# Kernel tuning notes

Hardware: AMD Instinct MI355X
Metric: run time of the kernel (lower is better)

The kernel has to match this reference:

```python
import jax, jax.numpy as jnp
import numpy as np

B, H, S, D = 2, 16, 2048, 64
DROPOUT_P = 0.1
INV_SCALE = 8.0  # sqrt(D), original: q.size(3) * k.size(-1)**-0.5


def setup_inputs() -> dict:
    key = jax.random.key(0)
    kq, kk, kv, km = jax.random.split(key, 4)
    query = jax.random.normal(kq, (B, H, S, D), dtype=jnp.float32)
    k_ = jax.random.normal(kk, (B, H, S, D), dtype=jnp.float32)
    value = jax.random.normal(kv, (B, H, S, D), dtype=jnp.float32)
    keep = jax.random.bernoulli(km, 1.0 - DROPOUT_P, (B, H, S, S))
    # torch train-mode dropout: keep-mask scaled by 1/(1-p)
    dropout_mask = keep.astype(jnp.float32) / (1.0 - DROPOUT_P)
    return {"query": query, "key": k_, "value": value, "dropout_mask": dropout_mask}


def reference(query, key, value, dropout_mask):
    # qk = q @ k^T, scaled by 1/sqrt(D)
    scores = jnp.einsum("bhqd,bhkd->bhqk", query, key) / INV_SCALE
    probs = jax.nn.softmax(scores, axis=-1)
    probs = probs * dropout_mask  # deterministic dropout
    out = jnp.einsum("bhqk,bhkd->bhqd", probs, value)
    return out
```

## Files before the change

### kernel.cpp

```cpp
#include <hip/hip_runtime.h>
#include <hip/hip_bf16.h>

typedef __attribute__((ext_vector_type(4))) float f32x4;
typedef __attribute__((ext_vector_type(8))) short s16x8;
typedef __attribute__((ext_vector_type(4))) short s16x4;

constexpr int S    = 2048;
constexpr int D    = 64;
constexpr int BH   = 32;
constexpr int QBLK = 64;
constexpr int KBLK = 32;
constexpr int NSL  = S / KBLK;

__device__ __forceinline__ short f2bf(float f) {
  union { float f; unsigned u; } x;
  x.f = f;
  unsigned r = x.u + 0x7fffu + ((x.u >> 16) & 1u);
  return (short)(r >> 16);
}

typedef const __attribute__((address_space(1))) unsigned int* as1_u32p;
typedef __attribute__((address_space(3))) unsigned int* as3_u32p;

__global__ __launch_bounds__(256) void prepass(const float* __restrict__ K,
                                               const float* __restrict__ V,
                                               short* __restrict__ Kb,
                                               short* __restrict__ Vt) {
  const int bid = blockIdx.x;
  const int tid = threadIdx.x;
  if (bid < BH * 32) {
    const int bh = bid >> 5, sl = bid & 31;
    const float* src = K + ((size_t)bh * S + (size_t)sl * 64) * D;
    short* dst = Kb + ((size_t)bh * S + (size_t)sl * 64) * D;
    #pragma unroll
    for (int c = 0; c < 2; ++c) {
      const int idx = tid * 2 + c;
      const int row = idx >> 3;
      const int ch  = idx & 7;
      const float* s = src + row * D + ch * 8;
      f32x4 a = *(const f32x4*)s, b = *(const f32x4*)(s + 4);
      s16x8 o;
      #pragma unroll
      for (int j = 0; j < 4; ++j) { o[j] = f2bf(a[j]); o[4 + j] = f2bf(b[j]); }
      *(s16x8*)(dst + row * D + ((ch ^ (row & 7)) * 8)) = o;
    }
  } else {
    __shared__ short tile[32][72];
    const int b2 = bid - BH * 32;
    const int bh = b2 >> 6, sl = b2 & 63;
    const float* src = V + ((size_t)bh * S + (size_t)sl * 32) * D;
    {
      const int row = tid >> 3;
      const int c0  = (tid & 7) * 8;
      f32x4 a = *(const f32x4*)(src + row * D + c0);
      f32x4 b = *(const f32x4*)(src + row * D + c0 + 4);
      #pragma unroll
      for (int j = 0; j < 4; ++j) {
        tile[row][c0 + j]     = f2bf(a[j]);
        tile[row][c0 + 4 + j] = f2bf(b[j]);
      }
    }
    __syncthreads();
    short* dst = Vt + ((size_t)bh * 64 + sl) * (D * KBLK);
    const int d = tid >> 2, c = tid & 3;
    const int pos = c ^ ((d >> 1) & 3);
    s16x8 o;
    #pragma unroll
    for (int j = 0; j < 8; ++j) o[j] = tile[c * 8 + j][d];
    *(s16x8*)(dst + d * KBLK + pos * 8) = o;
  }
}

__global__ __launch_bounds__(256, 4)
void attn_fwd4(const float* __restrict__ Qg, const short* __restrict__ Kb,
               const short* __restrict__ Vt, const float* __restrict__ Mg,
               float* __restrict__ Og) {
  __shared__ alignas(16) short K_lds[3][KBLK][64];
  __shared__ alignas(16) short V_lds[3][D][KBLK];
  __shared__ alignas(16) short P_lds[4][16][KBLK];

  const int tid  = threadIdx.x;
  const int wave = tid >> 6;
  const int lane = tid & 63;
  const int lq   = lane & 15;
  const int g    = lane >> 4;

  const int bh = blockIdx.x & (BH - 1);
  const int qt = blockIdx.x / BH;
  const size_t base = (size_t)bh * S * D;
  const int    qrow = qt * QBLK + wave * 16 + lq;
  const float* mrow = Mg + ((size_t)bh * S + qrow) * S + g * 4;

  s16x8 qf[2];
  {
    const float sc = 1.44269504088896340736f * 0.125f;
    const float* qp = Qg + base + (size_t)qrow * D + g * 8;
    #pragma unroll
    for (int h = 0; h < 2; ++h) {
      f32x4 a = *(const f32x4*)(qp + h * 32);
      f32x4 b = *(const f32x4*)(qp + h * 32 + 4);
      #pragma unroll
      for (int j = 0; j < 4; ++j) {
        qf[h][j]     = f2bf(a[j] * sc);
        qf[h][4 + j] = f2bf(b[j] * sc);
      }
    }
  }

  f32x4 acc[4];
  #pragma unroll
  for (int dt = 0; dt < 4; ++dt) acc[dt] = (f32x4)0.0f;
  float m = -1e30f, lp = 0.0f;

  const char* kbase = (const char*)(Kb + base);
  const char* vbase = (const char*)(Vt + (size_t)bh * 64 * (D * KBLK));
  char* kl = (char*)&K_lds[0][0][0];
  char* vl = (char*)&V_lds[0][0][0];
  char* pl = (char*)&P_lds[wave][lq][0];

  auto stageKV = [&](int buf, int it) {
    __builtin_amdgcn_global_load_lds((as1_u32p)(kbase + (size_t)it * 4096 + wave * 1024 + lane * 16),
                                     (as3_u32p)(kl + buf * 4096 + wave * 1024 + lane * 16), 16, 0, 0);
    __builtin_amdgcn_global_load_lds((as1_u32p)(vbase + (size_t)it * 4096 + wave * 1024 + lane * 16),
                                     (as3_u32p)(vl + buf * 4096 + wave * 1024 + lane * 16), 16, 0, 0);
  };
  auto loadM = [&](int it, f32x4* mk) {
    const float* mp = mrow + it * KBLK;
    mk[0] = *(const f32x4*)(mp);
    mk[1] = *(const f32x4*)(mp + 16);
  };

  auto body = [&](int it, int cur, f32x4* mkU, f32x4* mkN) {
    {
      int nb = cur + 2; if (nb >= 3) nb -= 3;
      if (it + 2 < NSL) stageKV(nb, it + 2);
      if (it + 1 < NSL) loadM(it + 1, mkN);
    }

    f32x4 st[2];
    __builtin_amdgcn_s_setprio(1);
    #pragma unroll
    for (int t = 0; t < 2; ++t) {
      st[t] = (f32x4)0.0f;
      #pragma unroll
      for (int h = 0; h < 2; ++h) {
        const s16x8 kf = *(const s16x8*)(kl + cur * 4096 + (t * 16 + lq) * 128 +
                                         (((h * 4 + g) ^ (lq & 7)) * 16));
        st[t] = __builtin_amdgcn_mfma_f32_16x16x32_bf16(kf, qf[h], st[t], 0, 0, 0);
      }
    }
    __builtin_amdgcn_s_setprio(0);

    const float mx = fmaxf(fmaxf(fmaxf(st[0][0], st[0][1]), fmaxf(st[0][2], st[0][3])),
                           fmaxf(fmaxf(st[1][0], st[1][1]), fmaxf(st[1][2], st[1][3])));
    if (!__all(mx <= m + 8.0f)) {
      float rm = fmaxf(mx, __shfl_xor(mx, 16));
      rm = fmaxf(rm, __shfl_xor(rm, 32));
      const float mn  = fmaxf(m, rm);
      const float fac = __builtin_amdgcn_exp2f(m - mn);
      lp *= fac;
      #pragma unroll
      for (int dt = 0; dt < 4; ++dt)
        #pragma unroll
        for (int r = 0; r < 4; ++r) acc[dt][r] *= fac;
      m = mn;
    }
    float p[8];
    #pragma unroll
    for (int t = 0; t < 2; ++t)
      #pragma unroll
      for (int r = 0; r < 4; ++r) p[t * 4 + r] = __builtin_amdgcn_exp2f(st[t][r] - m);
    lp += ((p[0] + p[1]) + (p[2] + p[3])) + ((p[4] + p[5]) + (p[6] + p[7]));

    #pragma unroll
    for (int t = 0; t < 2; ++t) {
      s16x4 pk;
      #pragma unroll
      for (int r = 0; r < 4; ++r) pk[r] = f2bf(p[t * 4 + r] * mkU[t][r]);
      *(s16x4*)(pl + (((2 * t + (g >> 1)) ^ ((lq >> 1) & 3)) * 16) + (g & 1) * 8) = pk;
    }
    asm volatile("" ::: "memory");

    const s16x8 pf = *(const s16x8*)(pl + ((g ^ ((lq >> 1) & 3)) * 16));
    __builtin_amdgcn_s_setprio(1);
    #pragma unroll
    for (int dt = 0; dt < 4; ++dt) {
      const s16x8 vf = *(const s16x8*)(vl + cur * 4096 + (dt * 16 + lq) * 64 +
                                       ((g ^ ((lq >> 1) & 3)) * 16));
      acc[dt] = __builtin_amdgcn_mfma_f32_16x16x32_bf16(vf, pf, acc[dt], 0, 0, 0);
    }
    __builtin_amdgcn_s_setprio(0);

    asm volatile("s_waitcnt vmcnt(4)" ::: "memory");
    __builtin_amdgcn_s_barrier();
    __builtin_amdgcn_sched_barrier(0);
  };

  f32x4 mkA[2], mkB[2];
  stageKV(0, 0);
  stageKV(1, 1);
  loadM(0, mkA);
  asm volatile("s_waitcnt vmcnt(4)" ::: "memory");
  __builtin_amdgcn_s_barrier();
  __builtin_amdgcn_sched_barrier(0);

  int cur = 0;
  #pragma unroll 1
  for (int it = 0; it < NSL; it += 2) {
    body(it,     cur, mkA, mkB); cur = (cur == 2) ? 0 : cur + 1;
    body(it + 1, cur, mkB, mkA); cur = (cur == 2) ? 0 : cur + 1;
  }

  float l = lp + __shfl_xor(lp, 16);
  l += __shfl_xor(l, 32);
  const float inv_l = 1.0f / l;
  float* op = Og + base + (size_t)qrow * D;
  #pragma unroll
  for (int dt = 0; dt < 4; ++dt) {
    f32x4 o;
    #pragma unroll
    for (int r = 0; r < 4; ++r) o[r] = acc[dt][r] * inv_l;
    *(f32x4*)(op + dt * 16 + g * 4) = o;
  }
}

__global__ __launch_bounds__(256, 4)
void attn_fwd_fb(const float* __restrict__ Qg, const float* __restrict__ Kg,
                 const float* __restrict__ Vg, const float* __restrict__ Mg,
                 float* __restrict__ Og) {
  __shared__ alignas(16) short Kl[32][72];
  __shared__ alignas(16) short Vl[D][40];
  __shared__ alignas(16) short Pl[4][16][40];
  const int tid = threadIdx.x, wave = tid >> 6, lane = tid & 63;
  const int lq = lane & 15, g = lane >> 4;
  const int bh = blockIdx.x & (BH - 1), qt = blockIdx.x / BH;
  const size_t base = (size_t)bh * S * D;
  const int qrow = qt * QBLK + wave * 16 + lq;
  const float* mrow = Mg + ((size_t)bh * S + qrow) * S;
  s16x8 qf[2];
  {
    const float sc = 1.44269504088896340736f * 0.125f;
    const float* qp = Qg + base + (size_t)qrow * D + g * 8;
    #pragma unroll
    for (int h = 0; h < 2; ++h) {
      f32x4 a = *(const f32x4*)(qp + h * 32);
      f32x4 b = *(const f32x4*)(qp + h * 32 + 4);
      #pragma unroll
      for (int j = 0; j < 4; ++j) { qf[h][j] = f2bf(a[j] * sc); qf[h][4 + j] = f2bf(b[j] * sc); }
    }
  }
  f32x4 acc[4];
  #pragma unroll
  for (int dt = 0; dt < 4; ++dt) acc[dt] = (f32x4)0.0f;
  float m = -1e30f, l = 0.0f;
  for (int kb = 0; kb < S; kb += 32) {
    f32x4 mk[2];
    #pragma unroll
    for (int t = 0; t < 2; ++t) mk[t] = *(const f32x4*)(mrow + kb + t * 16 + g * 4);
    __syncthreads();
    {
      const int row = tid >> 3, d0 = (tid & 7) * 8;
      const float* kp = Kg + base + (size_t)(kb + row) * D + d0;
      f32x4 a = *(const f32x4*)kp, b = *(const f32x4*)(kp + 4);
      s16x8 f;
      #pragma unroll
      for (int j = 0; j < 4; ++j) { f[j] = f2bf(a[j]); f[4 + j] = f2bf(b[j]); }
      *(s16x8*)&Kl[row][d0] = f;
    }
    {
      const int d = tid & 63, kk = (tid >> 6) * 8;
      const float* vp = Vg + base + (size_t)(kb + kk) * D + d;
      s16x8 f;
      #pragma unroll
      for (int j = 0; j < 8; ++j) f[j] = f2bf(vp[(size_t)j * D]);
      *(s16x8*)&Vl[d][kk] = f;
    }
    __syncthreads();
    f32x4 st[2];
    #pragma unroll
    for (int t = 0; t < 2; ++t) {
      st[t] = (f32x4)0.0f;
      #pragma unroll
      for (int h = 0; h < 2; ++h) {
        s16x8 kf = *(const s16x8*)&Kl[t * 16 + lq][h * 32 + g * 8];
        st[t] = __builtin_amdgcn_mfma_f32_16x16x32_bf16(kf, qf[h], st[t], 0, 0, 0);
      }
    }
    float mx = st[0][0];
    #pragma unroll
    for (int t = 0; t < 2; ++t)
      #pragma unroll
      for (int r = 0; r < 4; ++r) mx = fmaxf(mx, st[t][r]);
    mx = fmaxf(mx, __shfl_xor(mx, 16));
    mx = fmaxf(mx, __shfl_xor(mx, 32));
    const float mn = fmaxf(m, mx);
    const float fac = __builtin_amdgcn_exp2f(m - mn);
    float p[8], ps = 0.0f;
    #pragma unroll
    for (int t = 0; t < 2; ++t)
      #pragma unroll
      for (int r = 0; r < 4; ++r) { float e = __builtin_amdgcn_exp2f(st[t][r] - mn); p[t * 4 + r] = e; ps += e; }
    ps += __shfl_xor(ps, 16);
    ps += __shfl_xor(ps, 32);
    l = l * fac + ps; m = mn;
    #pragma unroll
    for (int dt = 0; dt < 4; ++dt)
      #pragma unroll
      for (int r = 0; r < 4; ++r) acc[dt][r] *= fac;
    #pragma unroll
    for (int t = 0; t < 2; ++t) {
      s16x4 pk;
      #pragma unroll
      for (int r = 0; r < 4; ++r) pk[r] = f2bf(p[t * 4 + r] * mk[t][r]);
      *(s16x4*)&Pl[wave][lq][t * 16 + g * 4] = pk;
    }
    asm volatile("" ::: "memory");
    s16x8 pf = *(const s16x8*)&Pl[wave][lq][g * 8];
    #pragma unroll
    for (int dt = 0; dt < 4; ++dt) {
      s16x8 vf = *(const s16x8*)&Vl[dt * 16 + lq][g * 8];
      acc[dt] = __builtin_amdgcn_mfma_f32_16x16x32_bf16(vf, pf, acc[dt], 0, 0, 0);
    }
  }
  const float inv_l = 1.0f / l;
  float* op = Og + base + (size_t)qrow * D;
  #pragma unroll
  for (int dt = 0; dt < 4; ++dt) {
    f32x4 o;
    #pragma unroll
    for (int r = 0; r < 4; ++r) o[r] = acc[dt][r] * inv_l;
    *(f32x4*)(op + dt * 16 + g * 4) = o;
  }
}

extern "C" void kernel_launch(void* const* d_in, const int* in_sizes, int n_in,
                              void* d_out, int out_size, void* d_ws, size_t ws_size,
                              hipStream_t stream) {
  const float* Q = (const float*)d_in[0];
  const float* K = (const float*)d_in[1];
  const float* V = (const float*)d_in[2];
  const float* M = (const float*)d_in[3];
  float* O = (float*)d_out;
  const size_t need = 2ull * BH * S * D * sizeof(short);
  if (ws_size >= need) {
    short* Kb = (short*)d_ws;
    short* Vt = Kb + (size_t)BH * S * D;
    prepass<<<BH * 32 + BH * 64, 256, 0, stream>>>(K, V, Kb, Vt);
    attn_fwd4<<<(S / QBLK) * BH, 256, 0, stream>>>(Q, Kb, Vt, M, O);
  } else {
    attn_fwd_fb<<<(S / QBLK) * BH, 256, 0, stream>>>(Q, K, V, M, O);
  }
}
```

Measured before the change: 176.1 us.

## Load K/V fragments directly from global into registers, dropping LDS staging and barriers

The prepass now writes K and V in a fragment-native layout, so each lane can load its MFMA operands straight from global memory with 16-byte loads. The attention kernel no longer stages K/V tiles into LDS and drops the per-iteration waitcnt and block barrier. K is double-buffered in registers one iteration ahead. Launch bounds drop to 3 blocks per CU to make room for the extra registers. The trade-off is that each of the four waves in a block re-reads the same K/V from global/L2 instead of sharing one LDS copy, and occupancy is lower.

```diff
diff --git a/kernel.cpp b/kernel.cpp
--- a/kernel.cpp
+++ b/kernel.cpp
@@ -18,9 +18,6 @@
   unsigned r = x.u + 0x7fffu + ((x.u >> 16) & 1u);
   return (short)(r >> 16);
 }
-
-typedef const __attribute__((address_space(1))) unsigned int* as1_u32p;
-typedef __attribute__((address_space(3))) unsigned int* as3_u32p;
 
 __global__ __launch_bounds__(256) void prepass(const float* __restrict__ K,
                                                const float* __restrict__ V,
@@ -31,7 +28,7 @@
   if (bid < BH * 32) {
     const int bh = bid >> 5, sl = bid & 31;
     const float* src = K + ((size_t)bh * S + (size_t)sl * 64) * D;
-    short* dst = Kb + ((size_t)bh * S + (size_t)sl * 64) * D;
+    short* dstb = Kb + (size_t)bh * S * D + (size_t)sl * 4096;
     #pragma unroll
     for (int c = 0; c < 2; ++c) {
       const int idx = tid * 2 + c;
@@ -42,7 +39,9 @@
       s16x8 o;
       #pragma unroll
       for (int j = 0; j < 4; ++j) { o[j] = f2bf(a[j]); o[4 + j] = f2bf(b[j]); }
-      *(s16x8*)(dst + row * D + ((ch ^ (row & 7)) * 8)) = o;
+      const int off = (row >> 5) * 2048 + (((row >> 4) & 1) * 2 + (ch >> 2)) * 512 +
+                      ((ch & 3) * 16 + (row & 15)) * 8;
+      *(s16x8*)(dstb + off) = o;
     }
   } else {
     __shared__ short tile[32][72];
@@ -61,22 +60,19 @@
       }
     }
     __syncthreads();
-    short* dst = Vt + ((size_t)bh * 64 + sl) * (D * KBLK);
+    short* dst = Vt + (size_t)bh * S * D + (size_t)sl * 2048;
     const int d = tid >> 2, c = tid & 3;
-    const int pos = c ^ ((d >> 1) & 3);
     s16x8 o;
     #pragma unroll
     for (int j = 0; j < 8; ++j) o[j] = tile[c * 8 + j][d];
-    *(s16x8*)(dst + d * KBLK + pos * 8) = o;
-  }
-}
-
-__global__ __launch_bounds__(256, 4)
-void attn_fwd4(const float* __restrict__ Qg, const short* __restrict__ Kb,
+    *(s16x8*)(dst + (d >> 4) * 512 + (c * 16 + (d & 15)) * 8) = o;
+  }
+}
+
+__global__ __launch_bounds__(256, 3)
+void attn_fwd5(const float* __restrict__ Qg, const short* __restrict__ Kb,
                const short* __restrict__ Vt, const float* __restrict__ Mg,
                float* __restrict__ Og) {
-  __shared__ alignas(16) short K_lds[3][KBLK][64];
-  __shared__ alignas(16) short V_lds[3][D][KBLK];
   __shared__ alignas(16) short P_lds[4][16][KBLK];
 
   const int tid  = threadIdx.x;
@@ -112,17 +108,14 @@
   for (int dt = 0; dt < 4; ++dt) acc[dt] = (f32x4)0.0f;
   float m = -1e30f, lp = 0.0f;
 
-  const char* kbase = (const char*)(Kb + base);
-  const char* vbase = (const char*)(Vt + (size_t)bh * 64 * (D * KBLK));
-  char* kl = (char*)&K_lds[0][0][0];
-  char* vl = (char*)&V_lds[0][0][0];
+  const short* kt = Kb + base + lane * 8;
+  const short* vt = Vt + base + lane * 8;
   char* pl = (char*)&P_lds[wave][lq][0];
 
-  auto stageKV = [&](int buf, int it) {
-    __builtin_amdgcn_global_load_lds((as1_u32p)(kbase + (size_t)it * 4096 + wave * 1024 + lane * 16),
-                                     (as3_u32p)(kl + buf * 4096 + wave * 1024 + lane * 16), 16, 0, 0);
-    __builtin_amdgcn_global_load_lds((as1_u32p)(vbase + (size_t)it * 4096 + wave * 1024 + lane * 16),
-                                     (as3_u32p)(vl + buf * 4096 + wave * 1024 + lane * 16), 16, 0, 0);
+  auto loadK = [&](int it, s16x8* kf) {
+    const short* p = kt + it * 2048;
+    #pragma unroll
+    for (int f = 0; f < 4; ++f) kf[f] = *(const s16x8*)(p + f * 512);
   };
   auto loadM = [&](int it, f32x4* mk) {
     const float* mp = mrow + it * KBLK;
@@ -130,11 +123,15 @@
     mk[1] = *(const f32x4*)(mp + 16);
   };
 
-  auto body = [&](int it, int cur, f32x4* mkU, f32x4* mkN) {
+  auto body = [&](int it, const s16x8* kfU, s16x8* kfN, const f32x4* mkU, f32x4* mkN) {
+    const int itn = (it + 1 < NSL) ? it + 1 : NSL - 1;
+    loadK(itn, kfN);
+    loadM(itn, mkN);
+    s16x8 vf[4];
     {
-      int nb = cur + 2; if (nb >= 3) nb -= 3;
-      if (it + 2 < NSL) stageKV(nb, it + 2);
-      if (it + 1 < NSL) loadM(it + 1, mkN);
+      const short* p = vt + it * 2048;
+      #pragma unroll
+      for (int dt = 0; dt < 4; ++dt) vf[dt] = *(const s16x8*)(p + dt * 512);
     }
 
     f32x4 st[2];
@@ -143,11 +140,8 @@
     for (int t = 0; t < 2; ++t) {
       st[t] = (f32x4)0.0f;
       #pragma unroll
-      for (int h = 0; h < 2; ++h) {
-        const s16x8 kf = *(const s16x8*)(kl + cur * 4096 + (t * 16 + lq) * 128 +
-                                         (((h * 4 + g) ^ (lq & 7)) * 16));
-        st[t] = __builtin_amdgcn_mfma_f32_16x16x32_bf16(kf, qf[h], st[t], 0, 0, 0);
-      }
+      for (int h = 0; h < 2; ++h)
+        st[t] = __builtin_amdgcn_mfma_f32_16x16x32_bf16(kfU[t * 2 + h], qf[h], st[t], 0, 0, 0);
     }
     __builtin_amdgcn_s_setprio(0);
 
@@ -180,35 +174,24 @@
       *(s16x4*)(pl + (((2 * t + (g >> 1)) ^ ((lq >> 1) & 3)) * 16) + (g & 1) * 8) = pk;
     }
     asm volatile("" ::: "memory");
-
     const s16x8 pf = *(const s16x8*)(pl + ((g ^ ((lq >> 1) & 3)) * 16));
+
     __builtin_amdgcn_s_setprio(1);
     #pragma unroll
-    for (int dt = 0; dt < 4; ++dt) {
-      const s16x8 vf = *(const s16x8*)(vl + cur * 4096 + (dt * 16 + lq) * 64 +
-                                       ((g ^ ((lq >> 1) & 3)) * 16));
-      acc[dt] = __builtin_amdgcn_mfma_f32_16x16x32_bf16(vf, pf, acc[dt], 0, 0, 0);
-    }
+    for (int dt = 0; dt < 4; ++dt)
+      acc[dt] = __builtin_amdgcn_mfma_f32_16x16x32_bf16(vf[dt], pf, acc[dt], 0, 0, 0);
     __builtin_amdgcn_s_setprio(0);
-
-    asm volatile("s_waitcnt vmcnt(4)" ::: "memory");
-    __builtin_amdgcn_s_barrier();
-    __builtin_amdgcn_sched_barrier(0);
   };
 
+  s16x8 kfA[4], kfB[4];
   f32x4 mkA[2], mkB[2];
-  stageKV(0, 0);
-  stageKV(1, 1);
+  loadK(0, kfA);
   loadM(0, mkA);
-  asm volatile("s_waitcnt vmcnt(4)" ::: "memory");
-  __builtin_amdgcn_s_barrier();
-  __builtin_amdgcn_sched_barrier(0);
-
-  int cur = 0;
+
   #pragma unroll 1
   for (int it = 0; it < NSL; it += 2) {
-    body(it,     cur, mkA, mkB); cur = (cur == 2) ? 0 : cur + 1;
-    body(it + 1, cur, mkB, mkA); cur = (cur == 2) ? 0 : cur + 1;
+    body(it,     kfA, kfB, mkA, mkB);
+    body(it + 1, kfB, kfA, mkB, mkA);
   }
 
   float l = lp + __shfl_xor(lp, 16);
@@ -346,7 +329,7 @@
     short* Kb = (short*)d_ws;
     short* Vt = Kb + (size_t)BH * S * D;
     prepass<<<BH * 32 + BH * 64, 256, 0, stream>>>(K, V, Kb, Vt);
-    attn_fwd4<<<(S / QBLK) * BH, 256, 0, stream>>>(Q, Kb, Vt, M, O);
+    attn_fwd5<<<(S / QBLK) * BH, 256, 0, stream>>>(Q, Kb, Vt, M, O);
   } else {
     attn_fwd_fb<<<(S / QBLK) * BH, 256, 0, stream>>>(Q, K, V, M, O);
   }
```

Measured after the change: 233.6 us. 32.7% more time.
